# Optimization experiments

Measured on AMD Instinct MI355X. Metric: run time of the kernel, lower is better.

The kernel has to match this reference:

```python
import jax, jax.numpy as jnp
import numpy as np
from jax import lax

DN = ('NHWC', 'HWIO', 'NHWC')


def _conv(x, w):
    # x: [B,H,W,Cin], w: [kh,kw,Cin,Cout], 'same' padding
    return lax.conv_general_dilated(x, w, (1, 1), 'SAME', dimension_numbers=DN)


def _hard_sigmoid(x):
    # Keras hard_sigmoid: clip(0.2*x + 0.5, 0, 1)
    return jnp.clip(0.2 * x + 0.5, 0.0, 1.0)


def convlstm2d(x, Wk, Uk, b, filters):
    """Keras ConvLSTM2D, return_sequences=True, padding='same'.
    x: [B,T,H,W,Cin]. Gate order in kernel: [i, f, c, o].
    Returns h sequence [B,T,H,W,filters].
    """
    B, T, H, W, _ = x.shape
    h0 = jnp.zeros((B, H, W, filters), x.dtype)
    c0 = jnp.zeros((B, H, W, filters), x.dtype)

    def step(carry, xt):
        h, c = carry
        z = _conv(xt, Wk) + _conv(h, Uk) + b  # [B,H,W,4*filters]
        zi, zf, zc, zo = jnp.split(z, 4, axis=-1)
        i = _hard_sigmoid(zi)
        f = _hard_sigmoid(zf)
        o = _hard_sigmoid(zo)
        c_new = f * c + i * jnp.tanh(zc)
        h_new = o * jnp.tanh(c_new)
        return (h_new, c_new), h_new

    xs = jnp.moveaxis(x, 1, 0)  # [T,B,H,W,Cin]
    _, hs = lax.scan(step, (h0, c0), xs)
    return jnp.moveaxis(hs, 0, 1)  # [B,T,H,W,filters]


def setup_inputs() -> dict:
    key = jax.random.key(0)
    ks = jax.random.split(key, 7)
    B, T, H, W, Cin, F = 8, 10, 64, 64, 32, 64
    s = 0.05
    return {
        'x': jax.random.normal(ks[0], (B, T, H, W, Cin), jnp.float32),
        'Wk1': jax.random.normal(ks[1], (5, 5, Cin, 4 * F), jnp.float32) * s,
        'Uk1': jax.random.normal(ks[2], (5, 5, F, 4 * F), jnp.float32) * s,
        'b1': jnp.zeros((4 * F,), jnp.float32),
        'Wk2': jax.random.normal(ks[3], (3, 3, F, 4 * F), jnp.float32) * s,
        'Uk2': jax.random.normal(ks[4], (3, 3, F, 4 * F), jnp.float32) * s,
        'b2': jnp.zeros((4 * F,), jnp.float32),
    }


def reference(x, Wk1, Uk1, b1, Wk2, Uk2, b2):
    F = Uk1.shape[2]
    y = jax.nn.relu(convlstm2d(x, Wk1, Uk1, b1, F))
    y = jax.nn.relu(convlstm2d(y, Wk2, Uk2, b2, F))
    return y
```

## Files before the change

kernel.cpp:

```cpp
#include <hip/hip_runtime.h>
#include <cstdint>
#include <cmath>


#define NT        256
#define NTU       256
#define RELU_BLKS 256

typedef __attribute__((ext_vector_type(8))) short short8;
typedef __attribute__((ext_vector_type(4))) float f32x4;

__device__ __forceinline__ float hsig(float v) {
    return fminf(fmaxf(fmaf(v, 0.2f, 0.5f), 0.0f), 1.0f);
}

__device__ __forceinline__ short bf16rnd(float f) {
    union { float f; unsigned u; } a; a.f = f;
    return (short)((a.u + 0x7FFFu + ((a.u >> 16) & 1u)) >> 16);
}

__device__ __forceinline__ void split_bf16(float f, short& h, short& l) {
    h = bf16rnd(f);
    union { unsigned u; float f; } b; b.u = ((unsigned)(unsigned short)h) << 16;
    l = bf16rnd(f - b.f);
}

__device__ __forceinline__ float from_bf16(short s) {
    union { unsigned u; float f; } b; b.u = ((unsigned)(unsigned short)s) << 16;
    return b.f;
}

struct BF { uint4 bh[4]; uint4 bl[4]; };

template<int CINX, int KS, bool WRITE_SEQ, bool HZ>
__device__ __forceinline__ void step_body(
    short* __restrict__ xs, short* __restrict__ hs,
    const short* __restrict__ xp, long xp_bstride,
    const short* __restrict__ h_prev,
    float* __restrict__ c_state,
    const short* __restrict__ Wpk,
    const short* __restrict__ Upk,
    const float* __restrict__ bias,
    short* __restrict__ h_next,
    short* __restrict__ seq, long seq_bstride,
    int bidx)
{
    constexpr int PAD  = KS / 2;
    constexpr int COLS = 64 + 2 * PAD;
    constexpr int CHX  = CINX / 32;
    constexpr int SEGS = HZ ? CHX : (CHX + 2);
    constexpr int PSTX = 2 * CINX + 8;
    constexpr int PSTH = 136;
    constexpr int VPPX = CINX / 4;

    const int tid  = threadIdx.x;
    const int lane = tid & 63;
    const int fg   = tid >> 6;
    const int q8   = ((lane >> 4) & 3) * 8;
    const int batch = bidx >> 6;
    const int y     = bidx & 63;

    const short* xim = xp + (size_t)batch * xp_bstride;
    const short* him = h_prev + (size_t)batch * 4096 * 128;

    for (int idx = tid; idx < (COLS * PSTX) / 8; idx += NT) {
        uint4 z; z.x = 0; z.y = 0; z.z = 0; z.w = 0;
        *(uint4*)(xs + idx * 8) = z;
    }
    if constexpr (!HZ) {
        for (int idx = tid; idx < (COLS * PSTH) / 8; idx += NT) {
            uint4 z; z.x = 0; z.y = 0; z.z = 0; z.w = 0;
            *(uint4*)(hs + idx * 8) = z;
        }
    }

    f32x4 acc[4][4];
    #pragma unroll
    for (int g = 0; g < 4; ++g)
        #pragma unroll
        for (int mt = 0; mt < 4; ++mt)
            #pragma unroll
            for (int r = 0; r < 4; ++r) acc[g][mt][r] = 0.0f;

    auto loadB = [&](int ky, int kx, int s) -> BF {
        int tap = ky * KS + kx;
        const short* base;
        if (s < CHX)
            base = Wpk + ((size_t)((tap * CHX + s) * 16 + fg)) * 1024 + lane * 16;
        else
            base = Upk + ((size_t)((tap * 2 + (s - CHX)) * 16 + fg)) * 1024 + lane * 16;
        BF b;
        #pragma unroll
        for (int g = 0; g < 4; ++g) {
            b.bh[g] = *(const uint4*)(base + (size_t)g * 4096);
            b.bl[g] = *(const uint4*)(base + (size_t)g * 4096 + 8);
        }
        return b;
    };

    const int ky0   = (y < PAD) ? (PAD - y) : 0;
    const int kyend = (64 + PAD - y) < KS ? (64 + PAD - y) : KS;

    BF bcur = loadB(ky0, 0, 0);

    for (int ky = ky0; ky < kyend; ++ky) {
        int yin = y + ky - PAD;
        __syncthreads();
        const short* xrow = xim + (size_t)yin * 64 * 2 * CINX;
        for (int idx = tid; idx < 64 * VPPX; idx += NT) {
            int px = idx / VPPX;
            int v  = idx - px * VPPX;
            *(uint4*)(xs + (px + PAD) * PSTX + v * 8)
                = *(const uint4*)(xrow + px * 2 * CINX + v * 8);
        }
        if constexpr (!HZ) {
            const short* hrow = him + (size_t)yin * 64 * 128;
            for (int idx = tid; idx < 64 * 16; idx += NT) {
                int px = idx >> 4;
                int v  = idx & 15;
                *(uint4*)(hs + (px + PAD) * PSTH + v * 8)
                    = *(const uint4*)(hrow + px * 128 + v * 8);
            }
        }
        __syncthreads();

        #pragma unroll
        for (int kx = 0; kx < KS; ++kx) {
            #pragma unroll
            for (int s = 0; s < SEGS; ++s) {
                int ns = s + 1, nkx = kx, nky = ky;
                if (ns == SEGS) { ns = 0; ++nkx; }
                if (nkx == KS)  { nkx = 0; ++nky; }
                nky = (nky < kyend) ? nky : ky;
                BF bnxt = loadB(nky, nkx, ns);

                short8 ah[4], al[4];
                #pragma unroll
                for (int mt = 0; mt < 4; ++mt) {
                    int col = mt * 16 + (lane & 15) + kx;
                    const short* p = (s < CHX)
                        ? (xs + col * PSTX + s * 32 + q8)
                        : (hs + col * PSTH + (s - CHX) * 32 + q8);
                    int lo = (s < CHX) ? CINX : 64;
                    ah[mt] = *(const short8*)p;
                    al[mt] = *(const short8*)(p + lo);
                }
                #pragma unroll
                for (int g = 0; g < 4; ++g) {
                    short8 bh = *(const short8*)&bcur.bh[g];
                    short8 bl = *(const short8*)&bcur.bl[g];
                    #pragma unroll
                    for (int mt = 0; mt < 4; ++mt) {
                        acc[g][mt] = __builtin_amdgcn_mfma_f32_16x16x32_bf16(
                            ah[mt], bh, acc[g][mt], 0, 0, 0);
                        acc[g][mt] = __builtin_amdgcn_mfma_f32_16x16x32_bf16(
                            al[mt], bh, acc[g][mt], 0, 0, 0);
                        acc[g][mt] = __builtin_amdgcn_mfma_f32_16x16x32_bf16(
                            ah[mt], bl, acc[g][mt], 0, 0, 0);
                    }
                }
                bcur = bnxt;
            }
        }
    }

    const int fl = fg * 16 + (lane & 15);
    const float b_i = bias[fl];
    const float b_f = bias[64 + fl];
    const float b_c = bias[128 + fl];
    const float b_o = bias[192 + fl];
    const int q = (lane >> 4) & 3;

    const long pixbase = (long)batch * 4096 + (long)y * 64;
    const long cb = pixbase * 64 + fl;
    const long sb = (long)batch * seq_bstride + ((long)y * 64) * 128 + fl;

    #pragma unroll
    for (int mt = 0; mt < 4; ++mt) {
        #pragma unroll
        for (int r = 0; r < 4; ++r) {
            int col = mt * 16 + q * 4 + r;
            long cidx = cb + (long)col * 64;
            float zi = acc[0][mt][r] + b_i;
            float zf = acc[1][mt][r] + b_f;
            float zc = acc[2][mt][r] + b_c;
            float zo = acc[3][mt][r] + b_o;
            float ig = hsig(zi);
            float fgt = hsig(zf);
            float og = hsig(zo);
            float cp = HZ ? 0.0f : c_state[cidx];
            float cn = fgt * cp + ig * tanhf(zc);
            float hn = og * tanhf(cn);
            c_state[cidx] = cn;

            short hh, hl;
            split_bf16(hn, hh, hl);
            long hoff = (pixbase + col) * 128 + fl;
            h_next[hoff]      = hh;
            h_next[hoff + 64] = hl;
            if (WRITE_SEQ) {
                bool pos = hn > 0.0f;
                seq[sb + (long)col * 128]      = pos ? hh : (short)0;
                seq[sb + (long)col * 128 + 64] = pos ? hl : (short)0;
            }
        }
    }
}

template<int CINX, int KS, bool WRITE_SEQ, bool HZ>
__global__ __launch_bounds__(NT, 2)
void convlstm_step(
    const short* __restrict__ xp, long xp_bstride,
    const short* __restrict__ h_prev,
    float* __restrict__ c_state,
    const short* __restrict__ Wpk,
    const short* __restrict__ Upk,
    const float* __restrict__ bias,
    short* __restrict__ h_next,
    short* __restrict__ seq, long seq_bstride)
{
    extern __shared__ __align__(16) short smem[];
    constexpr int PAD  = KS / 2;
    constexpr int COLS = 64 + 2 * PAD;
    constexpr int PSTX = 2 * CINX + 8;
    step_body<CINX, KS, WRITE_SEQ, HZ>(
        smem, smem + COLS * PSTX,
        xp, xp_bstride, h_prev, c_state, Wpk, Upk, bias,
        h_next, seq, seq_bstride, (int)blockIdx.x);
}

__global__ __launch_bounds__(NT, 3)
void convlstm_fused(
    const short* __restrict__ x1, long x1_bs,
    const short* __restrict__ h1p, float* __restrict__ c1,
    const short* __restrict__ Wp1, const short* __restrict__ Up1,
    const float* __restrict__ b1,
    short* __restrict__ h1n, short* __restrict__ seq1, long seq1_bs,
    const short* __restrict__ x2, long x2_bs,
    const short* __restrict__ h2p, float* __restrict__ c2,
    const short* __restrict__ Wp2, const short* __restrict__ Up2,
    const float* __restrict__ b2,
    short* __restrict__ h2n,
    const short* __restrict__ relu_src, float* __restrict__ relu_dst,
    long out_bstride)
{
    extern __shared__ __align__(16) short smem[];
    const int b = (int)blockIdx.x;
    if (b < 512) {
        step_body<32, 5, true, false>(
            smem, smem + 68 * 72,
            x1, x1_bs, h1p, c1, Wp1, Up1, b1, h1n, seq1, seq1_bs, b);
    } else if (b < 1024) {
        step_body<64, 3, false, false>(
            smem, smem + 66 * 136,
            x2, x2_bs, h2p, c2, Wp2, Up2, b2, h2n, nullptr, 0, b - 512);
    } else {
        if (relu_dst == nullptr) return;
        long i = (long)(b - 1024) * NT + threadIdx.x;
        for (; i < (1L << 21); i += (long)RELU_BLKS * NT) {
            long pix = i >> 6;
            int  c   = (int)(i & 63);
            float f = from_bf16(relu_src[pix * 128 + c])
                    + from_bf16(relu_src[pix * 128 + 64 + c]);
            long bb = pix >> 12;
            relu_dst[bb * out_bstride + (pix & 4095) * 64 + c] = fmaxf(f, 0.0f);
        }
    }
}

__global__ void convert_planes32(const float4* __restrict__ src,
                                 unsigned* __restrict__ dst, int n4)
{
    int t = blockIdx.x * NTU + threadIdx.x;
    if (t >= n4) return;
    int pix = t >> 3;
    int c4  = t & 7;
    float4 v = src[t];
    short h0, l0, h1, l1, h2, l2, h3, l3;
    split_bf16(v.x, h0, l0);
    split_bf16(v.y, h1, l1);
    split_bf16(v.z, h2, l2);
    split_bf16(v.w, h3, l3);
    unsigned* p = dst + (size_t)pix * 32;
    p[c4 * 2]      = (unsigned)(unsigned short)h0 | ((unsigned)(unsigned short)h1 << 16);
    p[c4 * 2 + 1]  = (unsigned)(unsigned short)h2 | ((unsigned)(unsigned short)h3 << 16);
    p[16 + c4 * 2]     = (unsigned)(unsigned short)l0 | ((unsigned)(unsigned short)l1 << 16);
    p[16 + c4 * 2 + 1] = (unsigned)(unsigned short)l2 | ((unsigned)(unsigned short)l3 << 16);
}

__global__ void repack(const float* __restrict__ src, short* __restrict__ dst,
                       int KS, int CH)
{
    int total = KS * KS * CH * 16 * 64;
    int t = blockIdx.x * NTU + threadIdx.x;
    if (t >= total) return;
    int u = t >> 6, lane = t & 63;
    int tap = u / (CH * 16);
    int rem = u - tap * (CH * 16);
    int ch = rem >> 4;
    int gfg = rem & 15;
    int g = gfg >> 2, fgp = gfg & 3;
    int CIN = CH * 32;
    int n = lane & 15, qq = lane >> 4;
    short* d = dst + (size_t)u * 1024 + lane * 16;
    int gc = g * 64 + fgp * 16 + n;
    for (int j = 0; j < 8; ++j) {
        int c = ch * 32 + qq * 8 + j;
        float w = src[((size_t)tap * CIN + c) * 256 + gc];
        short h, l;
        split_bf16(w, h, l);
        d[j] = h;
        d[8 + j] = l;
    }
}

__global__ void relu_copy(const short* __restrict__ hp, float* __restrict__ out,
                          long out_bstride)
{
    long i = (long)blockIdx.x * NTU + threadIdx.x;
    long pix = i >> 6;
    int c = (int)(i & 63);
    float f = from_bf16(hp[pix * 128 + c]) + from_bf16(hp[pix * 128 + 64 + c]);
    long b = pix >> 12;
    long within = (pix & 4095) * 64 + c;
    out[b * out_bstride + within] = fmaxf(f, 0.0f);
}

extern "C" void kernel_launch(void* const* d_in, const int* in_sizes, int n_in,
                              void* d_out, int out_size, void* d_ws, size_t ws_size,
                              hipStream_t stream) {
    const float* x   = (const float*)d_in[0];
    const float* Wk1 = (const float*)d_in[1];
    const float* Uk1 = (const float*)d_in[2];
    const float* b1  = (const float*)d_in[3];
    const float* Wk2 = (const float*)d_in[4];
    const float* Uk2 = (const float*)d_in[5];
    const float* b2  = (const float*)d_in[6];
    float* out = (float*)d_out;

    const long S  = (long)8 * 64 * 64 * 64;
    const long oT = (long)64 * 64 * 64;
    const long oB = 10 * oT;
    const long x1T = (long)4096 * 64;
    const long x1B = 10 * x1T;

    const size_t HB  = (size_t)4 * S;
    const size_t CB  = (size_t)4 * S;
    const size_t W1B = (size_t)25 * 1 * 16 * 1024 * 2;
    const size_t U1B = (size_t)25 * 2 * 16 * 1024 * 2;
    const size_t W2B = (size_t)9 * 2 * 16 * 1024 * 2;
    const size_t U2B = (size_t)9 * 2 * 16 * 1024 * 2;
    const size_t XPB = (size_t)8 * x1B * 2;
    const size_t need_ov = 4 * HB + 2 * CB + W1B + U1B + W2B + U2B + XPB;
    const bool ov = (ws_size >= need_ov);

    short* h1a = (short*)d_ws;
    short* h1b = h1a + 2 * S;
    short *h2a, *h2b;
    float *c1, *c2;
    short* Wp1;
    if (ov) {
        h2a = h1b + 2 * S;
        h2b = h2a + 2 * S;
        c1  = (float*)(h2b + 2 * S);
        c2  = c1 + S;
        Wp1 = (short*)(c2 + S);
    } else {
        h2a = h1a; h2b = h1b;
        c1  = (float*)(h1b + 2 * S);
        c2  = c1;
        Wp1 = (short*)(c1 + S);
    }
    short* Up1 = Wp1 + 25 * 1 * 16 * 1024;
    short* Wp2 = Up1 + 25 * 2 * 16 * 1024;
    short* Up2 = Wp2 + 9 * 2 * 16 * 1024;
    short* x1p = Up2 + 9 * 2 * 16 * 1024;

    {
        int n4 = 8 * 10 * 4096 * 8;
        convert_planes32<<<dim3((n4 + NTU - 1) / NTU), dim3(NTU), 0, stream>>>(
            (const float4*)x, (unsigned*)x1p, n4);
    }
    repack<<<dim3((25 * 1 * 16 * 64 + NTU - 1) / NTU), dim3(NTU), 0, stream>>>(Wk1, Wp1, 5, 1);
    repack<<<dim3((25 * 2 * 16 * 64 + NTU - 1) / NTU), dim3(NTU), 0, stream>>>(Uk1, Up1, 5, 2);
    repack<<<dim3((9 * 2 * 16 * 64 + NTU - 1) / NTU), dim3(NTU), 0, stream>>>(Wk2, Wp2, 3, 2);
    repack<<<dim3((9 * 2 * 16 * 64 + NTU - 1) / NTU), dim3(NTU), 0, stream>>>(Uk2, Up2, 3, 2);

    short* seqs = (short*)d_out;

    const size_t SH_L1HZ = (size_t)(68 * 72) * 2;
    const size_t SH_L1   = (size_t)(68 * 72 + 68 * 136) * 2;
    const size_t SH_L2   = (size_t)(66 * 136) * 4;
    const size_t SH_F    = SH_L2;

    if (ov) {
        hipMemsetAsync(h2a, 0, HB, stream);
        hipMemsetAsync(c2, 0, CB, stream);

        convlstm_step<32, 5, true, true><<<dim3(512), dim3(NT), SH_L1HZ, stream>>>(
            x1p, x1B, h1a, c1, Wp1, Up1, b1, h1b, seqs, oB * 2);

        short* hc1 = h1b; short* hn1 = h1a;
        short* hc2 = h2a; short* hn2 = h2b;
        for (int t = 1; t < 10; ++t) {
            const short* x2 = seqs + (size_t)(t - 1) * oT * 2;
            float* rdst = (t >= 2) ? (out + (size_t)(t - 2) * oT) : (float*)nullptr;
            convlstm_fused<<<dim3(1024 + RELU_BLKS), dim3(NT), SH_F, stream>>>(
                x1p + (size_t)t * x1T, x1B, hc1, c1, Wp1, Up1, b1, hn1,
                seqs + (size_t)t * oT * 2, oB * 2,
                x2, oB * 2, hc2, c2, Wp2, Up2, b2, hn2,
                hc2, rdst, oB);
            short* tmp;
            tmp = hc1; hc1 = hn1; hn1 = tmp;
            tmp = hc2; hc2 = hn2; hn2 = tmp;
        }
        convlstm_step<64, 3, false, false><<<dim3(512), dim3(NT), SH_L2, stream>>>(
            seqs + (size_t)9 * oT * 2, oB * 2, hc2, c2, Wp2, Up2, b2, hn2,
            nullptr, 0);
        relu_copy<<<dim3(8192), dim3(NTU), 0, stream>>>(hc2, out + 8 * oT, oB);
        relu_copy<<<dim3(8192), dim3(NTU), 0, stream>>>(hn2, out + 9 * oT, oB);
    } else {
        convlstm_step<32, 5, true, true><<<dim3(512), dim3(NT), SH_L1HZ, stream>>>(
            x1p, x1B, h1a, c1, Wp1, Up1, b1, h1b, seqs, oB * 2);
        short* hc = h1b; short* hn = h1a;
        for (int t = 1; t < 10; ++t) {
            convlstm_step<32, 5, true, false><<<dim3(512), dim3(NT), SH_L1, stream>>>(
                x1p + (size_t)t * x1T, x1B, hc, c1, Wp1, Up1, b1, hn,
                seqs + (size_t)t * oT * 2, oB * 2);
            short* tmp = hc; hc = hn; hn = tmp;
        }
        hipMemsetAsync(hc, 0, HB, stream);
        hipMemsetAsync(c2, 0, CB, stream);
        convlstm_step<64, 3, false, false><<<dim3(512), dim3(NT), SH_L2, stream>>>(
            seqs, oB * 2, hc, c2, Wp2, Up2, b2, hn, nullptr, 0);
        relu_copy<<<dim3(8192), dim3(NTU), 0, stream>>>(hn, out, oB);
        { short* tmp = hc; hc = hn; hn = tmp; }
        for (int t = 1; t < 10; ++t) {
            convlstm_step<64, 3, false, false><<<dim3(512), dim3(NT), SH_L2, stream>>>(
                seqs + (size_t)t * oT * 2, oB * 2, hc, c2, Wp2, Up2, b2, hn,
                nullptr, 0);
            relu_copy<<<dim3(8192), dim3(NTU), 0, stream>>>(hn, out + (size_t)t * oT, oB);
            short* tmp = hc; hc = hn; hn = tmp;
        }
    }
}
```

Before: 1.649 ms.

## Remap blocks so each XCD owns one batch; interleave layer blocks and fuse relu

Block indices are remapped so that consecutive blockIdx values, which round-robin across the 8 XCDs, give each XCD the tiles of a single batch image. Halo rows and the per-batch state then stay within one XCD's L2. In the fused kernel, layer-1 and layer-2 tiles are interleaved on each XCD, and the relu tail is split per batch to match. The final standalone relu_copy is folded into the last layer-2 step launch. This aims to improve L2 locality and overlap, but depends on the hardware dispatching blocks round-robin across XCDs.

After: 2.294 ms. 39.1% more time.

```diff
diff --git a/kernel.cpp b/kernel.cpp
--- a/kernel.cpp
+++ b/kernel.cpp
@@ -31,6 +31,21 @@
 }
 
 struct BF { uint4 bh[4]; uint4 bl[4]; };
+
+__device__ __forceinline__ void relu_tail(
+    int bat, int j, const short* __restrict__ relu_src,
+    float* __restrict__ relu_dst, long out_bstride)
+{
+    const long pbase = (long)bat * 4096;
+    for (long le = (long)j * NT + threadIdx.x; le < 262144; le += 32L * NT) {
+        long pr  = le >> 6;
+        int  c   = (int)(le & 63);
+        long pix = pbase + pr;
+        float f = from_bf16(relu_src[pix * 128 + c])
+                + from_bf16(relu_src[pix * 128 + 64 + c]);
+        relu_dst[(long)bat * out_bstride + pr * 64 + c] = fmaxf(f, 0.0f);
+    }
+}
 
 template<int CINX, int KS, bool WRITE_SEQ, bool HZ>
 __device__ __forceinline__ void step_body(
@@ -217,16 +232,26 @@
     const short* __restrict__ Upk,
     const float* __restrict__ bias,
     short* __restrict__ h_next,
-    short* __restrict__ seq, long seq_bstride)
+    short* __restrict__ seq, long seq_bstride,
+    const short* __restrict__ relu_src, float* __restrict__ relu_dst,
+    long out_bstride)
 {
     extern __shared__ __align__(16) short smem[];
+    const int i = (int)blockIdx.x;
+    if (i >= 512) {
+        if (relu_dst == nullptr) return;
+        const int ri = i - 512;
+        relu_tail(ri & 7, ri >> 3, relu_src, relu_dst, out_bstride);
+        return;
+    }
     constexpr int PAD  = KS / 2;
     constexpr int COLS = 64 + 2 * PAD;
     constexpr int PSTX = 2 * CINX + 8;
+    const int bidx = ((i & 7) << 6) | (i >> 3);
     step_body<CINX, KS, WRITE_SEQ, HZ>(
         smem, smem + COLS * PSTX,
         xp, xp_bstride, h_prev, c_state, Wpk, Upk, bias,
-        h_next, seq, seq_bstride, (int)blockIdx.x);
+        h_next, seq, seq_bstride, bidx);
 }
 
 __global__ __launch_bounds__(NT, 3)
@@ -245,26 +270,24 @@
     long out_bstride)
 {
     extern __shared__ __align__(16) short smem[];
-    const int b = (int)blockIdx.x;
-    if (b < 512) {
-        step_body<32, 5, true, false>(
-            smem, smem + 68 * 72,
-            x1, x1_bs, h1p, c1, Wp1, Up1, b1, h1n, seq1, seq1_bs, b);
-    } else if (b < 1024) {
-        step_body<64, 3, false, false>(
-            smem, smem + 66 * 136,
-            x2, x2_bs, h2p, c2, Wp2, Up2, b2, h2n, nullptr, 0, b - 512);
+    const int i = (int)blockIdx.x;
+    if (i < 1024) {
+        const int xcd  = i & 7;
+        const int slot = i >> 3;
+        const int w    = (xcd << 6) | (slot >> 1);
+        if ((slot & 1) == 0) {
+            step_body<32, 5, true, false>(
+                smem, smem + 68 * 72,
+                x1, x1_bs, h1p, c1, Wp1, Up1, b1, h1n, seq1, seq1_bs, w);
+        } else {
+            step_body<64, 3, false, false>(
+                smem, smem + 66 * 136,
+                x2, x2_bs, h2p, c2, Wp2, Up2, b2, h2n, nullptr, 0, w);
+        }
     } else {
         if (relu_dst == nullptr) return;
-        long i = (long)(b - 1024) * NT + threadIdx.x;
-        for (; i < (1L << 21); i += (long)RELU_BLKS * NT) {
-            long pix = i >> 6;
-            int  c   = (int)(i & 63);
-            float f = from_bf16(relu_src[pix * 128 + c])
-                    + from_bf16(relu_src[pix * 128 + 64 + c]);
-            long bb = pix >> 12;
-            relu_dst[bb * out_bstride + (pix & 4095) * 64 + c] = fmaxf(f, 0.0f);
-        }
+        const int ri = i - 1024;
+        relu_tail(ri & 7, ri >> 3, relu_src, relu_dst, out_bstride);
     }
 }
 
@@ -398,7 +421,8 @@
         hipMemsetAsync(c2, 0, CB, stream);
 
         convlstm_step<32, 5, true, true><<<dim3(512), dim3(NT), SH_L1HZ, stream>>>(
-            x1p, x1B, h1a, c1, Wp1, Up1, b1, h1b, seqs, oB * 2);
+            x1p, x1B, h1a, c1, Wp1, Up1, b1, h1b, seqs, oB * 2,
+            nullptr, nullptr, 0);
 
         short* hc1 = h1b; short* hn1 = h1a;
         short* hc2 = h2a; short* hn2 = h2b;
@@ -414,31 +438,32 @@
             tmp = hc1; hc1 = hn1; hn1 = tmp;
             tmp = hc2; hc2 = hn2; hn2 = tmp;
         }
-        convlstm_step<64, 3, false, false><<<dim3(512), dim3(NT), SH_L2, stream>>>(
+        convlstm_step<64, 3, false, false><<<dim3(512 + RELU_BLKS), dim3(NT), SH_L2, stream>>>(
             seqs + (size_t)9 * oT * 2, oB * 2, hc2, c2, Wp2, Up2, b2, hn2,
-            nullptr, 0);
-        relu_copy<<<dim3(8192), dim3(NTU), 0, stream>>>(hc2, out + 8 * oT, oB);
+            nullptr, 0, hc2, out + 8 * oT, oB);
         relu_copy<<<dim3(8192), dim3(NTU), 0, stream>>>(hn2, out + 9 * oT, oB);
     } else {
         convlstm_step<32, 5, true, true><<<dim3(512), dim3(NT), SH_L1HZ, stream>>>(
-            x1p, x1B, h1a, c1, Wp1, Up1, b1, h1b, seqs, oB * 2);
+            x1p, x1B, h1a, c1, Wp1, Up1, b1, h1b, seqs, oB * 2,
+            nullptr, nullptr, 0);
         short* hc = h1b; short* hn = h1a;
         for (int t = 1; t < 10; ++t) {
             convlstm_step<32, 5, true, false><<<dim3(512), dim3(NT), SH_L1, stream>>>(
                 x1p + (size_t)t * x1T, x1B, hc, c1, Wp1, Up1, b1, hn,
-                seqs + (size_t)t * oT * 2, oB * 2);
+                seqs + (size_t)t * oT * 2, oB * 2, nullptr, nullptr, 0);
             short* tmp = hc; hc = hn; hn = tmp;
         }
         hipMemsetAsync(hc, 0, HB, stream);
         hipMemsetAsync(c2, 0, CB, stream);
         convlstm_step<64, 3, false, false><<<dim3(512), dim3(NT), SH_L2, stream>>>(
-            seqs, oB * 2, hc, c2, Wp2, Up2, b2, hn, nullptr, 0);
+            seqs, oB * 2, hc, c2, Wp2, Up2, b2, hn, nullptr, 0,
+            nullptr, nullptr, 0);
         relu_copy<<<dim3(8192), dim3(NTU), 0, stream>>>(hn, out, oB);
         { short* tmp = hc; hc = hn; hn = tmp; }
         for (int t = 1; t < 10; ++t) {
             convlstm_step<64, 3, false, false><<<dim3(512), dim3(NT), SH_L2, stream>>>(
                 seqs + (size_t)t * oT * 2, oB * 2, hc, c2, Wp2, Up2, b2, hn,
-                nullptr, 0);
+                nullptr, 0, nullptr, nullptr, 0);
             relu_copy<<<dim3(8192), dim3(NTU), 0, stream>>>(hn, out + (size_t)t * oT, oB);
             short* tmp = hc; hc = hn; hn = tmp;
         }
```

## Fuse layer-2 ReLU output into step epilogue and ping-pong layer-1 sequence buffers

Applied to the files above, without the earlier changes.

Layer 2's step epilogue now writes relu(h) straight into the fp32 output, which removes the separate ReLU blocks inside the fused kernel and the two trailing relu_copy launches. Layer 1's split-bf16 sequence now goes to two ping-pong workspace buffers instead of being staged in the output tensor. The final layer-2 step no longer writes an h_next buffer. This needs a larger workspace for the overlapped path and adds runtime null-pointer branches in the epilogue.

Measured after the change: 1.650 ms (median of 2 runs). About the same (+0.1%).

```diff
diff --git a/kernel.cpp b/kernel.cpp
--- a/kernel.cpp
+++ b/kernel.cpp
@@ -5,7 +5,6 @@
 
 #define NT        256
 #define NTU       256
-#define RELU_BLKS 256
 
 typedef __attribute__((ext_vector_type(8))) short short8;
 typedef __attribute__((ext_vector_type(4))) float f32x4;
@@ -43,6 +42,7 @@
     const float* __restrict__ bias,
     short* __restrict__ h_next,
     short* __restrict__ seq, long seq_bstride,
+    float* __restrict__ outf, long outf_bs,
     int bidx)
 {
     constexpr int PAD  = KS / 2;
@@ -174,6 +174,7 @@
     const long pixbase = (long)batch * 4096 + (long)y * 64;
     const long cb = pixbase * 64 + fl;
     const long sb = (long)batch * seq_bstride + ((long)y * 64) * 128 + fl;
+    const long ob = (long)batch * outf_bs + ((long)y * 64) * 64 + fl;
 
     #pragma unroll
     for (int mt = 0; mt < 4; ++mt) {
@@ -193,16 +194,22 @@
             float hn = og * tanhf(cn);
             c_state[cidx] = cn;
 
-            short hh, hl;
-            split_bf16(hn, hh, hl);
-            long hoff = (pixbase + col) * 128 + fl;
-            h_next[hoff]      = hh;
-            h_next[hoff + 64] = hl;
+            if (h_next) {
+                short hh, hl;
+                split_bf16(hn, hh, hl);
+                long hoff = (pixbase + col) * 128 + fl;
+                h_next[hoff]      = hh;
+                h_next[hoff + 64] = hl;
+            }
             if (WRITE_SEQ) {
+                short hh, hl;
+                split_bf16(hn, hh, hl);
                 bool pos = hn > 0.0f;
                 seq[sb + (long)col * 128]      = pos ? hh : (short)0;
                 seq[sb + (long)col * 128 + 64] = pos ? hl : (short)0;
             }
+            if (outf)
+                outf[ob + (long)col * 64] = fmaxf(hn, 0.0f);
         }
     }
 }
@@ -217,7 +224,8 @@
     const short* __restrict__ Upk,
     const float* __restrict__ bias,
     short* __restrict__ h_next,
-    short* __restrict__ seq, long seq_bstride)
+    short* __restrict__ seq, long seq_bstride,
+    float* __restrict__ outf, long outf_bs)
 {
     extern __shared__ __align__(16) short smem[];
     constexpr int PAD  = KS / 2;
@@ -226,7 +234,7 @@
     step_body<CINX, KS, WRITE_SEQ, HZ>(
         smem, smem + COLS * PSTX,
         xp, xp_bstride, h_prev, c_state, Wpk, Upk, bias,
-        h_next, seq, seq_bstride, (int)blockIdx.x);
+        h_next, seq, seq_bstride, outf, outf_bs, (int)blockIdx.x);
 }
 
 __global__ __launch_bounds__(NT, 3)
@@ -241,30 +249,20 @@
     const short* __restrict__ Wp2, const short* __restrict__ Up2,
     const float* __restrict__ b2,
     short* __restrict__ h2n,
-    const short* __restrict__ relu_src, float* __restrict__ relu_dst,
-    long out_bstride)
+    float* __restrict__ outf2, long outf2_bs)
 {
     extern __shared__ __align__(16) short smem[];
     const int b = (int)blockIdx.x;
     if (b < 512) {
         step_body<32, 5, true, false>(
             smem, smem + 68 * 72,
-            x1, x1_bs, h1p, c1, Wp1, Up1, b1, h1n, seq1, seq1_bs, b);
-    } else if (b < 1024) {
+            x1, x1_bs, h1p, c1, Wp1, Up1, b1, h1n, seq1, seq1_bs,
+            nullptr, 0, b);
+    } else {
         step_body<64, 3, false, false>(
             smem, smem + 66 * 136,
-            x2, x2_bs, h2p, c2, Wp2, Up2, b2, h2n, nullptr, 0, b - 512);
-    } else {
-        if (relu_dst == nullptr) return;
-        long i = (long)(b - 1024) * NT + threadIdx.x;
-        for (; i < (1L << 21); i += (long)RELU_BLKS * NT) {
-            long pix = i >> 6;
-            int  c   = (int)(i & 63);
-            float f = from_bf16(relu_src[pix * 128 + c])
-                    + from_bf16(relu_src[pix * 128 + 64 + c]);
-            long bb = pix >> 12;
-            relu_dst[bb * out_bstride + (pix & 4095) * 64 + c] = fmaxf(f, 0.0f);
-        }
+            x2, x2_bs, h2p, c2, Wp2, Up2, b2, h2n, nullptr, 0,
+            outf2, outf2_bs, b - 512);
     }
 }
 
@@ -343,6 +341,7 @@
     const long oB = 10 * oT;
     const long x1T = (long)4096 * 64;
     const long x1B = 10 * x1T;
+    const long sqB = (long)4096 * 128;
 
     const size_t HB  = (size_t)4 * S;
     const size_t CB  = (size_t)4 * S;
@@ -351,7 +350,7 @@
     const size_t W2B = (size_t)9 * 2 * 16 * 1024 * 2;
     const size_t U2B = (size_t)9 * 2 * 16 * 1024 * 2;
     const size_t XPB = (size_t)8 * x1B * 2;
-    const size_t need_ov = 4 * HB + 2 * CB + W1B + U1B + W2B + U2B + XPB;
+    const size_t need_ov = 6 * HB + 2 * CB + W1B + U1B + W2B + U2B + XPB;
     const bool ov = (ws_size >= need_ov);
 
     short* h1a = (short*)d_ws;
@@ -375,6 +374,8 @@
     short* Wp2 = Up1 + 25 * 2 * 16 * 1024;
     short* Up2 = Wp2 + 9 * 2 * 16 * 1024;
     short* x1p = Up2 + 9 * 2 * 16 * 1024;
+    short* sqA = x1p + 8 * x1B;
+    short* sqB_ = sqA + 2 * S;
 
     {
         int n4 = 8 * 10 * 4096 * 8;
@@ -386,8 +387,6 @@
     repack<<<dim3((9 * 2 * 16 * 64 + NTU - 1) / NTU), dim3(NTU), 0, stream>>>(Wk2, Wp2, 3, 2);
     repack<<<dim3((9 * 2 * 16 * 64 + NTU - 1) / NTU), dim3(NTU), 0, stream>>>(Uk2, Up2, 3, 2);
 
-    short* seqs = (short*)d_out;
-
     const size_t SH_L1HZ = (size_t)(68 * 72) * 2;
     const size_t SH_L1   = (size_t)(68 * 72 + 68 * 136) * 2;
     const size_t SH_L2   = (size_t)(66 * 136) * 4;
@@ -398,47 +397,49 @@
         hipMemsetAsync(c2, 0, CB, stream);
 
         convlstm_step<32, 5, true, true><<<dim3(512), dim3(NT), SH_L1HZ, stream>>>(
-            x1p, x1B, h1a, c1, Wp1, Up1, b1, h1b, seqs, oB * 2);
+            x1p, x1B, h1a, c1, Wp1, Up1, b1, h1b, sqA, sqB,
+            nullptr, 0);
 
         short* hc1 = h1b; short* hn1 = h1a;
         short* hc2 = h2a; short* hn2 = h2b;
         for (int t = 1; t < 10; ++t) {
-            const short* x2 = seqs + (size_t)(t - 1) * oT * 2;
-            float* rdst = (t >= 2) ? (out + (size_t)(t - 2) * oT) : (float*)nullptr;
-            convlstm_fused<<<dim3(1024 + RELU_BLKS), dim3(NT), SH_F, stream>>>(
+            short* seq_w = (t & 1) ? sqB_ : sqA;
+            short* seq_r = (t & 1) ? sqA : sqB_;
+            convlstm_fused<<<dim3(1024), dim3(NT), SH_F, stream>>>(
                 x1p + (size_t)t * x1T, x1B, hc1, c1, Wp1, Up1, b1, hn1,
-                seqs + (size_t)t * oT * 2, oB * 2,
-                x2, oB * 2, hc2, c2, Wp2, Up2, b2, hn2,
-                hc2, rdst, oB);
+                seq_w, sqB,
+                seq_r, sqB, hc2, c2, Wp2, Up2, b2, hn2,
+                out + (size_t)(t - 1) * oT, oB);
             short* tmp;
             tmp = hc1; hc1 = hn1; hn1 = tmp;
             tmp = hc2; hc2 = hn2; hn2 = tmp;
         }
         convlstm_step<64, 3, false, false><<<dim3(512), dim3(NT), SH_L2, stream>>>(
-            seqs + (size_t)9 * oT * 2, oB * 2, hc2, c2, Wp2, Up2, b2, hn2,
+            sqB_, sqB, hc2, c2, Wp2, Up2, b2, nullptr,
+            nullptr, 0, out + (size_t)9 * oT, oB);
+    } else {
+        short* seqs = (short*)d_out;
+        convlstm_step<32, 5, true, true><<<dim3(512), dim3(NT), SH_L1HZ, stream>>>(
+            x1p, x1B, h1a, c1, Wp1, Up1, b1, h1b, seqs, oB * 2,
             nullptr, 0);
-        relu_copy<<<dim3(8192), dim3(NTU), 0, stream>>>(hc2, out + 8 * oT, oB);
-        relu_copy<<<dim3(8192), dim3(NTU), 0, stream>>>(hn2, out + 9 * oT, oB);
-    } else {
-        convlstm_step<32, 5, true, true><<<dim3(512), dim3(NT), SH_L1HZ, stream>>>(
-            x1p, x1B, h1a, c1, Wp1, Up1, b1, h1b, seqs, oB * 2);
         short* hc = h1b; short* hn = h1a;
         for (int t = 1; t < 10; ++t) {
             convlstm_step<32, 5, true, false><<<dim3(512), dim3(NT), SH_L1, stream>>>(
                 x1p + (size_t)t * x1T, x1B, hc, c1, Wp1, Up1, b1, hn,
-                seqs + (size_t)t * oT * 2, oB * 2);
+                seqs + (size_t)t * oT * 2, oB * 2, nullptr, 0);
             short* tmp = hc; hc = hn; hn = tmp;
         }
         hipMemsetAsync(hc, 0, HB, stream);
         hipMemsetAsync(c2, 0, CB, stream);
         convlstm_step<64, 3, false, false><<<dim3(512), dim3(NT), SH_L2, stream>>>(
-            seqs, oB * 2, hc, c2, Wp2, Up2, b2, hn, nullptr, 0);
+            seqs, oB * 2, hc, c2, Wp2, Up2, b2, hn, nullptr, 0,
+            nullptr, 0);
         relu_copy<<<dim3(8192), dim3(NTU), 0, stream>>>(hn, out, oB);
         { short* tmp = hc; hc = hn; hn = tmp; }
         for (int t = 1; t < 10; ++t) {
             convlstm_step<64, 3, false, false><<<dim3(512), dim3(NT), SH_L2, stream>>>(
                 seqs + (size_t)t * oT * 2, oB * 2, hc, c2, Wp2, Up2, b2, hn,
-                nullptr, 0);
+                nullptr, 0, nullptr, 0);
             relu_copy<<<dim3(8192), dim3(NTU), 0, stream>>>(hn, out + (size_t)t * oT, oB);
             short* tmp = hc; hc = hn; hn = tmp;
         }
```
